# Optimization experiments

Hardware: AMD Instinct MI355X
Metric: run time of the kernel (lower is better)

## Reference

```python
import jax, jax.numpy as jnp
import numpy as np

N_NODES = 50000
N_EDGES = 800000
HIDDEN = 100
NUM_TASKS = 128
NUM_GRAPHS = 2000
ATOM_DIMS = [119, 5, 12, 12, 10, 6, 6, 2, 2]  # OGB full_atom_feature_dims
EPS = 1e-16  # stands in for PyG's clamp(min=0) so that pow(-1) stays finite


def setup_inputs() -> dict:
    key = jax.random.key(0)
    ks = jax.random.split(key, 8)
    x = jax.random.randint(ks[0], (N_NODES, 9), 0, 2, dtype=jnp.int32)
    edge_index = jax.random.randint(ks[1], (2, N_EDGES), 0, N_NODES, dtype=jnp.int32)
    batch = jnp.sort(jax.random.randint(ks[2], (N_NODES,), 0, NUM_GRAPHS, dtype=jnp.int32))
    s = 1.0 / np.sqrt(HIDDEN)
    atom_emb = jax.random.normal(ks[3], (sum(ATOM_DIMS), HIDDEN), jnp.float32)
    W1 = jax.random.normal(ks[4], (HIDDEN, HIDDEN), jnp.float32) * s
    b1 = jnp.zeros((HIDDEN,), jnp.float32)
    W2 = jax.random.normal(ks[5], (HIDDEN, HIDDEN), jnp.float32) * s
    b2 = jnp.zeros((HIDDEN,), jnp.float32)
    Wlin = jax.random.normal(ks[6], (HIDDEN, NUM_TASKS), jnp.float32) * s
    blin = jnp.zeros((NUM_TASKS,), jnp.float32)
    return dict(x=x, edge_index=edge_index, batch=batch, atom_emb=atom_emb,
                W1=W1, b1=b1, W2=W2, b2=b2, Wlin=Wlin, blin=blin)


def reference(x, edge_index, batch, atom_emb, W1, b1, W2, b2, Wlin, blin):
    # --- AtomEncoder: sum of per-feature categorical embeddings ---
    offsets = jnp.asarray(np.concatenate([[0], np.cumsum(ATOM_DIMS)[:-1]]), jnp.int32)
    h = jnp.take(atom_emb, x + offsets[None, :], axis=0).sum(axis=1)  # [N, H]

    # --- GCN normalization with self-loops (gcn_norm, edge_weight=None) ---
    loops = jnp.arange(N_NODES, dtype=edge_index.dtype)
    row = jnp.concatenate([edge_index[0], loops])  # source
    col = jnp.concatenate([edge_index[1], loops])  # target
    ew = jnp.ones(row.shape[0], jnp.float32)
    deg = jax.ops.segment_sum(ew, col, num_segments=N_NODES)  # in-degree incl self-loop
    dinv = jnp.where(deg > 0, deg ** -0.5, 0.0)
    norm = dinv[row] * ew * dinv[col]  # [E+N]
    cnt = jnp.maximum(deg, 1.0)  # messages per target node (for mean)

    def gcn_conv(h, W, b):
        msg = norm[:, None] * (h @ W)[row]  # [E+N, H]
        # PowerMeanAggregation(p=-1): clamp(0,100).pow(-1) -> mean -> clamp(0,100).pow(-1)
        msg = jnp.clip(msg, EPS, 100.0) ** (-1.0)
        agg = jax.ops.segment_sum(msg, col, num_segments=N_NODES) / cnt[:, None]
        return jnp.clip(agg, EPS, 100.0) ** (-1.0) + b

    h = jax.nn.relu(gcn_conv(h, W1, b1))
    h = gcn_conv(h, W2, b2)

    # --- global_mean_pool over batch ---
    gcnt = jax.ops.segment_sum(jnp.ones((N_NODES,), jnp.float32), batch, num_segments=NUM_GRAPHS)
    pooled = jax.ops.segment_sum(h, batch, num_segments=NUM_GRAPHS) / jnp.maximum(gcnt, 1.0)[:, None]

    return pooled @ Wlin + blin  # [NUM_GRAPHS, NUM_TASKS]
```

## Files before the change

### kernel.cpp

```cpp
#include <hip/hip_runtime.h>

#define N_NODES   50000
#define N_EDGES   800000
#define HIDDEN    100
#define NUM_TASKS 128
#define NUM_GRAPHS 2000
#define EPS 1e-16f

static __device__ __forceinline__ float rcp_fast(float v) {
    return __builtin_amdgcn_rcpf(v);
}
static __device__ __forceinline__ float invclip(float v) {
    return rcp_fast(fminf(fmaxf(v, EPS), 100.0f));
}
static __device__ __forceinline__ unsigned pack_bf16x2(float a, float b) {
    unsigned r;
    asm("v_cvt_pk_bf16_f32 %0, %1, %2" : "=v"(r) : "v"(a), "v"(b));
    return r;
}

__global__ void deg_count_kernel(const int* __restrict__ col, int* __restrict__ deg) {
    int e = blockIdx.x * blockDim.x + threadIdx.x;
    if (e < N_EDGES) atomicAdd(&deg[col[e]], 1);
}

__global__ void blk_sum_kernel(const int* __restrict__ deg, int* __restrict__ bsum) {
    int i = blockIdx.x * 256 + threadIdx.x;
    int v = (i < N_NODES) ? deg[i] : 0;
#pragma unroll
    for (int off = 32; off > 0; off >>= 1) v += __shfl_down(v, off, 64);
    __shared__ int ws[4];
    if ((threadIdx.x & 63) == 0) ws[threadIdx.x >> 6] = v;
    __syncthreads();
    if (threadIdx.x == 0) bsum[blockIdx.x] = ws[0] + ws[1] + ws[2] + ws[3];
}

__global__ void bsum_scan_kernel(int* __restrict__ bsum, int nblk) {
    __shared__ int buf[256];
    int t = threadIdx.x;
    int v = (t < nblk) ? bsum[t] : 0;
    buf[t] = v;
    __syncthreads();
    for (int off = 1; off < 256; off <<= 1) {
        int x = (t >= off) ? buf[t - off] : 0;
        __syncthreads();
        buf[t] += x;
        __syncthreads();
    }
    if (t < nblk) bsum[t] = buf[t] - v;
}

__global__ void blk_scan_kernel(const int* __restrict__ deg, const int* __restrict__ bbase,
                                int* __restrict__ csr_off, float* __restrict__ dinv,
                                int* __restrict__ cursor) {
    __shared__ int buf[256];
    int t = threadIdx.x;
    int i = blockIdx.x * 256 + t;
    int dv = (i < N_NODES) ? deg[i] : 0;
    buf[t] = dv;
    __syncthreads();
    for (int off = 1; off < 256; off <<= 1) {
        int x = (t >= off) ? buf[t - off] : 0;
        __syncthreads();
        buf[t] += x;
        __syncthreads();
    }
    if (i < N_NODES) {
        csr_off[i] = bbase[blockIdx.x] + buf[t] - dv;
        dinv[i] = 1.0f / sqrtf((float)(dv + 1));
        cursor[i] = 0;
    } else if (i == N_NODES) {
        csr_off[N_NODES] = N_EDGES;
    }
}

__global__ void scatter_kernel(const int* __restrict__ row, const int* __restrict__ col,
                               const int* __restrict__ csr_off, int* __restrict__ cursor,
                               const float* __restrict__ dinv, int2* __restrict__ csr_pack) {
    int e = blockIdx.x * blockDim.x + threadIdx.x;
    if (e >= N_EDGES) return;
    int s = row[e], d = col[e];
    int pos = csr_off[d] + atomicAdd(&cursor[d], 1);
    int2 p;
    p.x = s;
    p.y = __float_as_int(dinv[s] * dinv[d]);
    csr_pack[pos] = p;
}

__global__ void encoder_kernel(const int* __restrict__ x, const float* __restrict__ emb,
                               float* __restrict__ h) {
    int n = blockIdx.x;
    int d = threadIdx.x;
    if (d >= HIDDEN) return;
    const int offs[9] = {0, 119, 124, 136, 148, 158, 164, 170, 172};
    float acc = 0.0f;
#pragma unroll
    for (int f = 0; f < 9; ++f) {
        int idx = x[n * 9 + f] + offs[f];
        acc += emb[idx * HIDDEN + d];
    }
    h[n * HIDDEN + d] = acc;
}

#define MM_NODES 64
__global__ __launch_bounds__(512) void matmul_kernel(const float* __restrict__ h,
                                                     const float* __restrict__ W,
                                                     unsigned* __restrict__ outb) {
    __shared__ float hl[MM_NODES * HIDDEN];
    int tid = threadIdx.x;
    int nb = blockIdx.x * MM_NODES;

    for (int i = tid; i < MM_NODES * HIDDEN; i += 512) {
        int n = i / HIDDEN;
        hl[i] = (nb + n < N_NODES) ? h[(size_t)(nb + n) * HIDDEN + (i % HIDDEN)] : 0.0f;
    }
    __syncthreads();

    int tx = tid & 31;
    int txc = (tx < 25) ? tx : 24;
    int ty = tid >> 5;

    float4 acc[4];
#pragma unroll
    for (int jn = 0; jn < 4; ++jn) acc[jn] = make_float4(0.f, 0.f, 0.f, 0.f);

    for (int kk = 0; kk < HIDDEN; kk += 4) {
        float hs[4][4];
#pragma unroll
        for (int jn = 0; jn < 4; ++jn) {
            float4 hv = *(const float4*)&hl[(ty + 16 * jn) * HIDDEN + kk];
            hs[jn][0] = hv.x; hs[jn][1] = hv.y; hs[jn][2] = hv.z; hs[jn][3] = hv.w;
        }
#pragma unroll
        for (int dk = 0; dk < 4; ++dk) {
            float4 wv = *(const float4*)&W[(size_t)(kk + dk) * HIDDEN + 4 * txc];
#pragma unroll
            for (int jn = 0; jn < 4; ++jn) {
                acc[jn].x += hs[jn][dk] * wv.x;
                acc[jn].y += hs[jn][dk] * wv.y;
                acc[jn].z += hs[jn][dk] * wv.z;
                acc[jn].w += hs[jn][dk] * wv.w;
            }
        }
    }

    if (tx < 25) {
#pragma unroll
        for (int jn = 0; jn < 4; ++jn) {
            int n = nb + ty + 16 * jn;
            if (n < N_NODES) {
                uint2 pk;
                pk.x = pack_bf16x2(acc[jn].x, acc[jn].y);
                pk.y = pack_bf16x2(acc[jn].z, acc[jn].w);
                *(uint2*)&outb[(size_t)n * 50 + 2 * tx] = pk;
            }
        }
    }
}

__global__ __launch_bounds__(256) void agg_kernel(
        const unsigned* __restrict__ hw16, const int* __restrict__ csr_off,
        const int2* __restrict__ csr_pack, const float* __restrict__ dinv,
        const int* __restrict__ deg, const float* __restrict__ bias,
        float* __restrict__ out, int relu) {
    int wid  = (blockIdx.x * blockDim.x + threadIdx.x) >> 6;
    int lane = threadIdx.x & 63;
    if (wid >= N_NODES) return;
    int n = wid;
    bool act = lane < 50;

    float cnt = (float)(deg[n] + 1);
    float dn  = dinv[n];
    float nrm = dn * dn;

    float2 acc = make_float2(0.f, 0.f);
    if (act) {
        unsigned u = hw16[(size_t)n * 50 + lane];
        acc.x = invclip(nrm * __int_as_float(u << 16));
        acc.y = invclip(nrm * __int_as_float(u & 0xFFFF0000u));
    }

    int beg = csr_off[n], end = csr_off[n + 1];
    int i = beg;
    for (; i + 4 <= end; i += 4) {
        int2 p0 = csr_pack[i];
        int2 p1 = csr_pack[i + 1];
        int2 p2 = csr_pack[i + 2];
        int2 p3 = csr_pack[i + 3];
        unsigned u0 = act ? hw16[(size_t)p0.x * 50 + lane] : 0u;
        unsigned u1 = act ? hw16[(size_t)p1.x * 50 + lane] : 0u;
        unsigned u2 = act ? hw16[(size_t)p2.x * 50 + lane] : 0u;
        unsigned u3 = act ? hw16[(size_t)p3.x * 50 + lane] : 0u;
        float w0 = __int_as_float(p0.y), w1 = __int_as_float(p1.y);
        float w2 = __int_as_float(p2.y), w3 = __int_as_float(p3.y);
        acc.x += invclip(w0 * __int_as_float(u0 << 16));
        acc.y += invclip(w0 * __int_as_float(u0 & 0xFFFF0000u));
        acc.x += invclip(w1 * __int_as_float(u1 << 16));
        acc.y += invclip(w1 * __int_as_float(u1 & 0xFFFF0000u));
        acc.x += invclip(w2 * __int_as_float(u2 << 16));
        acc.y += invclip(w2 * __int_as_float(u2 & 0xFFFF0000u));
        acc.x += invclip(w3 * __int_as_float(u3 << 16));
        acc.y += invclip(w3 * __int_as_float(u3 & 0xFFFF0000u));
    }
    for (; i < end; ++i) {
        int2 p = csr_pack[i];
        unsigned u = act ? hw16[(size_t)p.x * 50 + lane] : 0u;
        float w = __int_as_float(p.y);
        acc.x += invclip(w * __int_as_float(u << 16));
        acc.y += invclip(w * __int_as_float(u & 0xFFFF0000u));
    }

    if (act) {
        float rcnt = rcp_fast(cnt);
        float2 o;
        o.x = invclip(acc.x * rcnt) + bias[2 * lane];
        o.y = invclip(acc.y * rcnt) + bias[2 * lane + 1];
        if (relu) { o.x = fmaxf(o.x, 0.f); o.y = fmaxf(o.y, 0.f); }
        *(float2*)&out[(size_t)n * HIDDEN + 2 * lane] = o;
    }
}

__global__ void pool_final_kernel(const float* __restrict__ h, const int* __restrict__ batch,
                                  const float* __restrict__ Wlin, const float* __restrict__ blin,
                                  float* __restrict__ out) {
    int g = blockIdx.x;
    int t = threadIdx.x;
    __shared__ float pl[HIDDEN];

    int lo = 0, hi = N_NODES;
    while (lo < hi) { int mid = (lo + hi) >> 1; if (batch[mid] < g) lo = mid + 1; else hi = mid; }
    int start = lo;
    hi = N_NODES;
    while (lo < hi) { int mid = (lo + hi) >> 1; if (batch[mid] < g + 1) lo = mid + 1; else hi = mid; }
    int end = lo;

    float inv = 1.0f / fmaxf((float)(end - start), 1.0f);
    if (t < HIDDEN) {
        float acc = 0.f;
        for (int n = start; n < end; ++n) acc += h[(size_t)n * HIDDEN + t];
        pl[t] = acc * inv;
    }
    __syncthreads();

    float o = 0.f;
#pragma unroll 4
    for (int j = 0; j < HIDDEN; ++j) o += pl[j] * Wlin[j * NUM_TASKS + t];
    out[(size_t)g * NUM_TASKS + t] = o + blin[t];
}

extern "C" void kernel_launch(void* const* d_in, const int* in_sizes, int n_in,
                              void* d_out, int out_size, void* d_ws, size_t ws_size,
                              hipStream_t stream) {
    const int*   x     = (const int*)d_in[0];
    const int*   ei    = (const int*)d_in[1];
    const int*   batch = (const int*)d_in[2];
    const float* emb   = (const float*)d_in[3];
    const float* W1    = (const float*)d_in[4];
    const float* b1    = (const float*)d_in[5];
    const float* W2    = (const float*)d_in[6];
    const float* b2    = (const float*)d_in[7];
    const float* Wlin  = (const float*)d_in[8];
    const float* blin  = (const float*)d_in[9];
    float* out = (float*)d_out;

    const int* row = ei;
    const int* col = ei + N_EDGES;

    char* ws = (char*)d_ws;
    auto alloc = [&](size_t bytes) -> char* {
        char* p = ws;
        ws += (bytes + 255) & ~(size_t)255;
        return p;
    };
    int*      deg      = (int*)     alloc((size_t)N_NODES * 4);
    int*      cursor   = (int*)     alloc((size_t)N_NODES * 4);
    int*      csr_off  = (int*)     alloc((size_t)(N_NODES + 1) * 4);
    float*    dinv     = (float*)   alloc((size_t)N_NODES * 4);
    int2*     csr_pack = (int2*)    alloc((size_t)N_EDGES * 8);
    float*    bufA     = (float*)   alloc((size_t)N_NODES * HIDDEN * 4);
    unsigned* hw16     = (unsigned*)alloc((size_t)N_NODES * 50 * 4);
    int*      bsum     = (int*)     alloc(256 * 4);

    const int SCAN_BLOCKS = (N_NODES + 255) / 256;

    hipMemsetAsync(deg, 0, (size_t)N_NODES * 4, stream);
    deg_count_kernel<<<(N_EDGES + 255) / 256, 256, 0, stream>>>(col, deg);
    blk_sum_kernel<<<SCAN_BLOCKS, 256, 0, stream>>>(deg, bsum);
    bsum_scan_kernel<<<1, 256, 0, stream>>>(bsum, SCAN_BLOCKS);
    blk_scan_kernel<<<SCAN_BLOCKS, 256, 0, stream>>>(deg, bsum, csr_off, dinv, cursor);
    scatter_kernel<<<(N_EDGES + 255) / 256, 256, 0, stream>>>(row, col, csr_off, cursor, dinv,
                                                              csr_pack);
    encoder_kernel<<<N_NODES, 128, 0, stream>>>(x, emb, bufA);

    const int MM_BLOCKS = (N_NODES + MM_NODES - 1) / MM_NODES;
    matmul_kernel<<<MM_BLOCKS, 512, 0, stream>>>(bufA, W1, hw16);
    agg_kernel<<<(N_NODES + 3) / 4, 256, 0, stream>>>(hw16, csr_off, csr_pack,
                                                      dinv, deg, b1, bufA, 1);
    matmul_kernel<<<MM_BLOCKS, 512, 0, stream>>>(bufA, W2, hw16);
    agg_kernel<<<(N_NODES + 3) / 4, 256, 0, stream>>>(hw16, csr_off, csr_pack,
                                                      dinv, deg, b2, bufA, 0);

    pool_final_kernel<<<NUM_GRAPHS, 128, 0, stream>>>(bufA, batch, Wlin, blin, out);
}
```

Measured before the change: 309.1 us.

## Use bf16 MFMA for dense transforms and store intermediate activations as bf16

```diff
diff --git a/kernel.cpp b/kernel.cpp
--- a/kernel.cpp
+++ b/kernel.cpp
@@ -7,6 +7,10 @@
 #define NUM_GRAPHS 2000
 #define EPS 1e-16f
 
+typedef unsigned short u16;
+typedef __attribute__((ext_vector_type(8))) short bf16x8;
+typedef __attribute__((ext_vector_type(4))) float f32x4;
+
 static __device__ __forceinline__ float rcp_fast(float v) {
     return __builtin_amdgcn_rcpf(v);
 }
@@ -18,6 +22,8 @@
     asm("v_cvt_pk_bf16_f32 %0, %1, %2" : "=v"(r) : "v"(a), "v"(b));
     return r;
 }
+static __device__ __forceinline__ float bf_lo(unsigned u) { return __int_as_float(u << 16); }
+static __device__ __forceinline__ float bf_hi(unsigned u) { return __int_as_float(u & 0xFFFF0000u); }
 
 __global__ void deg_count_kernel(const int* __restrict__ col, int* __restrict__ deg) {
     int e = blockIdx.x * blockDim.x + threadIdx.x;
@@ -88,72 +94,91 @@
 }
 
 __global__ void encoder_kernel(const int* __restrict__ x, const float* __restrict__ emb,
-                               float* __restrict__ h) {
+                               unsigned* __restrict__ hb) {
     int n = blockIdx.x;
-    int d = threadIdx.x;
-    if (d >= HIDDEN) return;
+    int t = threadIdx.x;
+    if (t >= 50) return;
     const int offs[9] = {0, 119, 124, 136, 148, 158, 164, 170, 172};
-    float acc = 0.0f;
+    float a0 = 0.f, a1 = 0.f;
 #pragma unroll
     for (int f = 0; f < 9; ++f) {
         int idx = x[n * 9 + f] + offs[f];
-        acc += emb[idx * HIDDEN + d];
-    }
-    h[n * HIDDEN + d] = acc;
-}
-
-#define MM_NODES 64
-__global__ __launch_bounds__(512) void matmul_kernel(const float* __restrict__ h,
-                                                     const float* __restrict__ W,
-                                                     unsigned* __restrict__ outb) {
-    __shared__ float hl[MM_NODES * HIDDEN];
+        float2 v = *(const float2*)&emb[(size_t)idx * HIDDEN + 2 * t];
+        a0 += v.x; a1 += v.y;
+    }
+    hb[(size_t)n * 50 + t] = pack_bf16x2(a0, a1);
+}
+
+#define MMB  64
+#define LDSK 152
+__global__ __launch_bounds__(256) void mfma_matmul_kernel(
+        const unsigned* __restrict__ inb, const float* __restrict__ W,
+        unsigned* __restrict__ outb) {
+    __shared__ u16 lds[(MMB + 112) * LDSK];
+    u16* A_l  = lds;
+    u16* Bt_l = lds + MMB * LDSK;
+    float* C_l = (float*)(lds + MMB * LDSK);
     int tid = threadIdx.x;
-    int nb = blockIdx.x * MM_NODES;
-
-    for (int i = tid; i < MM_NODES * HIDDEN; i += 512) {
-        int n = i / HIDDEN;
-        hl[i] = (nb + n < N_NODES) ? h[(size_t)(nb + n) * HIDDEN + (i % HIDDEN)] : 0.0f;
-    }
-    __syncthreads();
-
-    int tx = tid & 31;
-    int txc = (tx < 25) ? tx : 24;
-    int ty = tid >> 5;
-
-    float4 acc[4];
-#pragma unroll
-    for (int jn = 0; jn < 4; ++jn) acc[jn] = make_float4(0.f, 0.f, 0.f, 0.f);
-
-    for (int kk = 0; kk < HIDDEN; kk += 4) {
-        float hs[4][4];
-#pragma unroll
-        for (int jn = 0; jn < 4; ++jn) {
-            float4 hv = *(const float4*)&hl[(ty + 16 * jn) * HIDDEN + kk];
-            hs[jn][0] = hv.x; hs[jn][1] = hv.y; hs[jn][2] = hv.z; hs[jn][3] = hv.w;
-        }
-#pragma unroll
-        for (int dk = 0; dk < 4; ++dk) {
-            float4 wv = *(const float4*)&W[(size_t)(kk + dk) * HIDDEN + 4 * txc];
-#pragma unroll
-            for (int jn = 0; jn < 4; ++jn) {
-                acc[jn].x += hs[jn][dk] * wv.x;
-                acc[jn].y += hs[jn][dk] * wv.y;
-                acc[jn].z += hs[jn][dk] * wv.z;
-                acc[jn].w += hs[jn][dk] * wv.w;
-            }
-        }
-    }
-
-    if (tx < 25) {
-#pragma unroll
-        for (int jn = 0; jn < 4; ++jn) {
-            int n = nb + ty + 16 * jn;
-            if (n < N_NODES) {
-                uint2 pk;
-                pk.x = pack_bf16x2(acc[jn].x, acc[jn].y);
-                pk.y = pack_bf16x2(acc[jn].z, acc[jn].w);
-                *(uint2*)&outb[(size_t)n * 50 + 2 * tx] = pk;
-            }
+    int nb  = blockIdx.x * MMB;
+
+    for (int i = tid; i < MMB * 25; i += 256) {
+        int n = i / 25, j = i % 25;
+        uint2 v = make_uint2(0u, 0u);
+        if (nb + n < N_NODES) v = *(const uint2*)&inb[(size_t)(nb + n) * 50 + 2 * j];
+        *(uint2*)&A_l[n * LDSK + 4 * j] = v;
+    }
+    for (int i = tid; i < MMB * 7; i += 256) {
+        int n = i / 7, j = i % 7;
+        *(uint2*)&A_l[n * LDSK + 100 + 4 * j] = make_uint2(0u, 0u);
+    }
+    for (int i = tid; i < 112 * 64; i += 256) {
+        int n = i >> 6, kp = i & 63;
+        int k = 2 * kp;
+        float x0 = 0.f, x1 = 0.f;
+        if (n < HIDDEN) {
+            if (k < HIDDEN)     x0 = W[(size_t)k * HIDDEN + n];
+            if (k + 1 < HIDDEN) x1 = W[(size_t)(k + 1) * HIDDEN + n];
+        }
+        *(unsigned*)&Bt_l[n * LDSK + k] = pack_bf16x2(x0, x1);
+    }
+    __syncthreads();
+
+    int w = tid >> 6, l = tid & 63;
+    int mrow = 16 * w + (l & 15);
+    int koff = (l >> 4) * 8;
+
+    f32x4 acc[7];
+#pragma unroll
+    for (int t = 0; t < 7; ++t) acc[t] = (f32x4){0.f, 0.f, 0.f, 0.f};
+
+#pragma unroll
+    for (int ks = 0; ks < 4; ++ks) {
+        int k0 = 32 * ks + koff;
+        bf16x8 a = *(const bf16x8*)&A_l[mrow * LDSK + k0];
+#pragma unroll
+        for (int t = 0; t < 7; ++t) {
+            bf16x8 b = *(const bf16x8*)&Bt_l[(16 * t + (l & 15)) * LDSK + k0];
+            acc[t] = __builtin_amdgcn_mfma_f32_16x16x32_bf16(a, b, acc[t], 0, 0, 0);
+        }
+    }
+
+    __syncthreads();
+#pragma unroll
+    for (int t = 0; t < 7; ++t) {
+#pragma unroll
+        for (int r = 0; r < 4; ++r) {
+            int m = 16 * w + (l >> 4) * 4 + r;
+            C_l[m * 114 + 16 * t + (l & 15)] = acc[t][r];
+        }
+    }
+    __syncthreads();
+
+    for (int i = tid; i < MMB * 50; i += 256) {
+        int n = i / 50, d = i % 50;
+        if (nb + n < N_NODES) {
+            float xv = C_l[n * 114 + 2 * d];
+            float yv = C_l[n * 114 + 2 * d + 1];
+            outb[(size_t)(nb + n) * 50 + d] = pack_bf16x2(xv, yv);
         }
     }
 }
@@ -162,7 +187,7 @@
         const unsigned* __restrict__ hw16, const int* __restrict__ csr_off,
         const int2* __restrict__ csr_pack, const float* __restrict__ dinv,
         const int* __restrict__ deg, const float* __restrict__ bias,
-        float* __restrict__ out, int relu) {
+        unsigned* __restrict__ out16, float* __restrict__ out32, int relu) {
     int wid  = (blockIdx.x * blockDim.x + threadIdx.x) >> 6;
     int lane = threadIdx.x & 63;
     if (wid >= N_NODES) return;
@@ -176,8 +201,8 @@
     float2 acc = make_float2(0.f, 0.f);
     if (act) {
         unsigned u = hw16[(size_t)n * 50 + lane];
-        acc.x = invclip(nrm * __int_as_float(u << 16));
-        acc.y = invclip(nrm * __int_as_float(u & 0xFFFF0000u));
+        acc.x = invclip(nrm * bf_lo(u));
+        acc.y = invclip(nrm * bf_hi(u));
     }
 
     int beg = csr_off[n], end = csr_off[n + 1];
@@ -193,30 +218,29 @@
         unsigned u3 = act ? hw16[(size_t)p3.x * 50 + lane] : 0u;
         float w0 = __int_as_float(p0.y), w1 = __int_as_float(p1.y);
         float w2 = __int_as_float(p2.y), w3 = __int_as_float(p3.y);
-        acc.x += invclip(w0 * __int_as_float(u0 << 16));
-        acc.y += invclip(w0 * __int_as_float(u0 & 0xFFFF0000u));
-        acc.x += invclip(w1 * __int_as_float(u1 << 16));
-        acc.y += invclip(w1 * __int_as_float(u1 & 0xFFFF0000u));
-        acc.x += invclip(w2 * __int_as_float(u2 << 16));
-        acc.y += invclip(w2 * __int_as_float(u2 & 0xFFFF0000u));
-        acc.x += invclip(w3 * __int_as_float(u3 << 16));
-        acc.y += invclip(w3 * __int_as_float(u3 & 0xFFFF0000u));
+        acc.x += invclip(w0 * bf_lo(u0)); acc.y += invclip(w0 * bf_hi(u0));
+        acc.x += invclip(w1 * bf_lo(u1)); acc.y += invclip(w1 * bf_hi(u1));
+        acc.x += invclip(w2 * bf_lo(u2)); acc.y += invclip(w2 * bf_hi(u2));
+        acc.x += invclip(w3 * bf_lo(u3)); acc.y += invclip(w3 * bf_hi(u3));
     }
     for (; i < end; ++i) {
         int2 p = csr_pack[i];
         unsigned u = act ? hw16[(size_t)p.x * 50 + lane] : 0u;
         float w = __int_as_float(p.y);
-        acc.x += invclip(w * __int_as_float(u << 16));
-        acc.y += invclip(w * __int_as_float(u & 0xFFFF0000u));
+        acc.x += invclip(w * bf_lo(u));
+        acc.y += invclip(w * bf_hi(u));
     }
 
     if (act) {
         float rcnt = rcp_fast(cnt);
-        float2 o;
-        o.x = invclip(acc.x * rcnt) + bias[2 * lane];
-        o.y = invclip(acc.y * rcnt) + bias[2 * lane + 1];
-        if (relu) { o.x = fmaxf(o.x, 0.f); o.y = fmaxf(o.y, 0.f); }
-        *(float2*)&out[(size_t)n * HIDDEN + 2 * lane] = o;
+        float ox = invclip(acc.x * rcnt) + bias[2 * lane];
+        float oy = invclip(acc.y * rcnt) + bias[2 * lane + 1];
+        if (relu) {
+            ox = fmaxf(ox, 0.f); oy = fmaxf(oy, 0.f);
+            out16[(size_t)n * 50 + lane] = pack_bf16x2(ox, oy);
+        } else {
+            *(float2*)&out32[(size_t)n * HIDDEN + 2 * lane] = make_float2(ox, oy);
+        }
     }
 }
 
@@ -277,8 +301,9 @@
     int*      csr_off  = (int*)     alloc((size_t)(N_NODES + 1) * 4);
     float*    dinv     = (float*)   alloc((size_t)N_NODES * 4);
     int2*     csr_pack = (int2*)    alloc((size_t)N_EDGES * 8);
+    unsigned* bufP     = (unsigned*)alloc((size_t)N_NODES * 50 * 4);
+    unsigned* hw16     = (unsigned*)alloc((size_t)N_NODES * 50 * 4);
     float*    bufA     = (float*)   alloc((size_t)N_NODES * HIDDEN * 4);
-    unsigned* hw16     = (unsigned*)alloc((size_t)N_NODES * 50 * 4);
     int*      bsum     = (int*)     alloc(256 * 4);
 
     const int SCAN_BLOCKS = (N_NODES + 255) / 256;
@@ -290,15 +315,15 @@
     blk_scan_kernel<<<SCAN_BLOCKS, 256, 0, stream>>>(deg, bsum, csr_off, dinv, cursor);
     scatter_kernel<<<(N_EDGES + 255) / 256, 256, 0, stream>>>(row, col, csr_off, cursor, dinv,
                                                               csr_pack);
-    encoder_kernel<<<N_NODES, 128, 0, stream>>>(x, emb, bufA);
-
-    const int MM_BLOCKS = (N_NODES + MM_NODES - 1) / MM_NODES;
-    matmul_kernel<<<MM_BLOCKS, 512, 0, stream>>>(bufA, W1, hw16);
+    encoder_kernel<<<N_NODES, 64, 0, stream>>>(x, emb, bufP);
+
+    const int MM_BLOCKS = (N_NODES + MMB - 1) / MMB;
+    mfma_matmul_kernel<<<MM_BLOCKS, 256, 0, stream>>>(bufP, W1, hw16);
     agg_kernel<<<(N_NODES + 3) / 4, 256, 0, stream>>>(hw16, csr_off, csr_pack,
-                                                      dinv, deg, b1, bufA, 1);
-    matmul_kernel<<<MM_BLOCKS, 512, 0, stream>>>(bufA, W2, hw16);
+                                                      dinv, deg, b1, bufP, nullptr, 1);
+    mfma_matmul_kernel<<<MM_BLOCKS, 256, 0, stream>>>(bufP, W2, hw16);
     agg_kernel<<<(N_NODES + 3) / 4, 256, 0, stream>>>(hw16, csr_off, csr_pack,
-                                                      dinv, deg, b2, bufA, 0);
+                                                      dinv, deg, b2, nullptr, bufA, 0);
 
     pool_final_kernel<<<NUM_GRAPHS, 128, 0, stream>>>(bufA, batch, Wlin, blin, out);
 }
```

Result: no change. 308.5 us (-0.2%).
